# Performance work log

Measured on AMD Instinct MI355X. Metric: run time of the kernel, lower is better.

The kernel has to match this reference:

```python
import jax, jax.numpy as jnp
import numpy as np

D_MODEL = 1024
N_HEADS = 16
D_HEAD = D_MODEL // N_HEADS
RANK = 128
N_COMPRESS = 64
STATE_DIM = 64
B_SZ = 2
S_LEN = 2048


def setup_inputs() -> dict:
    key = jax.random.key(0)
    ks = jax.random.split(key, 12)
    x = jax.random.normal(ks[0], (B_SZ, S_LEN, D_MODEL), dtype=jnp.float32)
    A = jax.random.normal(ks[1], (STATE_DIM, STATE_DIM), dtype=jnp.float32) * 0.01
    B_ssm = jax.random.normal(ks[2], (D_MODEL, STATE_DIM), dtype=jnp.float32) * 0.01
    W_imp = jax.random.normal(ks[3], (D_MODEL, STATE_DIM), dtype=jnp.float32) * 0.02   # Linear(state_dim->d_model), weight [out,in]
    W_router = jax.random.normal(ks[4], (N_COMPRESS, D_MODEL), dtype=jnp.float32) * 0.02
    compress_neurons = jax.random.normal(ks[5], (N_COMPRESS, D_MODEL, RANK), dtype=jnp.float32) * 0.02
    Wq = jax.random.normal(ks[6], (D_MODEL, RANK), dtype=jnp.float32) * 0.02
    Wk = jax.random.normal(ks[7], (D_MODEL, RANK), dtype=jnp.float32) * 0.02
    Wv = jax.random.normal(ks[8], (D_MODEL, RANK), dtype=jnp.float32) * 0.02
    Wo = jax.random.normal(ks[9], (D_MODEL, D_MODEL), dtype=jnp.float32) * 0.02
    mask = jnp.tril(jnp.ones((S_LEN, S_LEN), dtype=bool))[None, None]  # [1,1,S,S] causal
    return {"x": x, "A": A, "B_ssm": B_ssm, "W_imp": W_imp, "W_router": W_router,
            "compress_neurons": compress_neurons, "Wq": Wq, "Wk": Wk, "Wv": Wv,
            "Wo": Wo, "mask": mask}


def reference(x, A, B_ssm, W_imp, W_router, compress_neurons, Wq, Wk, Wv, Wo, mask):
    Bn, S, D = x.shape
    # ---- SSM: h_t = h_{t-1} @ A + x_t @ B (only final state is used) ----
    xB = jnp.einsum('bsd,dn->bsn', x, B_ssm)  # precompute input projection

    def step(h, u):
        h = h @ A + u
        return h, None

    h0 = jnp.zeros((Bn, STATE_DIM), dtype=x.dtype)
    h_final, _ = jax.lax.scan(step, h0, jnp.swapaxes(xB, 0, 1))  # scan over S

    h_proj = h_final @ W_imp.T                       # [B, d_model]
    importance = jax.nn.softmax(jnp.einsum('bsd,bd->bs', x, h_proj), axis=-1)

    # ---- Routing ----
    token_pref = jax.nn.softmax(x @ W_router.T, axis=-1)          # [B,S,n_compress]
    nw = jnp.einsum('bs,bsn->bn', importance, token_pref)         # [B,n_compress]
    nw = nw / (nw.sum(axis=-1, keepdims=True) + 1e-8)

    # ---- Shared compression -> QKV ----
    shared_compress = jnp.einsum('bn,ndr->bdr', nw, compress_neurons)  # [B,D,rank]
    hcomp = jnp.einsum('bsd,bdr->bsr', x, shared_compress)             # [B,S,rank]
    Q = (hcomp @ Wq.T).reshape(Bn, S, N_HEADS, D_HEAD).transpose(0, 2, 1, 3)
    K = (hcomp @ Wk.T).reshape(Bn, S, N_HEADS, D_HEAD).transpose(0, 2, 1, 3)
    V = (hcomp @ Wv.T).reshape(Bn, S, N_HEADS, D_HEAD).transpose(0, 2, 1, 3)

    scores = jnp.einsum('bhqd,bhkd->bhqk', Q, K) / np.sqrt(D_HEAD).astype(x.dtype)
    scores = jnp.where(mask, scores, jnp.array(-jnp.inf, dtype=scores.dtype))
    attn = jax.nn.softmax(scores, axis=-1)
    attn_out = jnp.einsum('bhqk,bhkd->bhqd', attn, V)
    attn_out = attn_out.transpose(0, 2, 1, 3).reshape(Bn, S, D_MODEL)
    output = attn_out @ Wo.T
    return output
```

## Files before the change

### kernel.cpp

```cpp
#include <hip/hip_runtime.h>
#include <hip/hip_bf16.h>

typedef __bf16 bf16x8 __attribute__((ext_vector_type(8)));
typedef float  f32x4  __attribute__((ext_vector_type(4)));
typedef float  f32x16 __attribute__((ext_vector_type(16)));
typedef unsigned int uint4v __attribute__((ext_vector_type(4)));

__device__ __forceinline__ unsigned short f2bf(float f){
  union { float f; unsigned int u; } v; v.f = f;
  unsigned int r = (v.u + 0x7FFFu + ((v.u >> 16) & 1u)) >> 16;
  return (unsigned short)r;
}

__device__ __forceinline__ float bf2f(unsigned short u){
  union { unsigned int i; float f; } v; v.i = ((unsigned int)u) << 16; return v.f;
}

__device__ __forceinline__ unsigned pkbf(float a, float b){
  unsigned r;
  asm("v_cvt_pk_bf16_f32 %0, %1, %2" : "=v"(r) : "v"(a), "v"(b));
  return r;
}

__device__ __forceinline__ void gload_lds16(const void* g, void* l){
  __builtin_amdgcn_global_load_lds(
      (const __attribute__((address_space(1))) unsigned int*)g,
      (__attribute__((address_space(3))) unsigned int*)l, 16, 0, 0);
}

#define MFMA16(a,b,c) __builtin_amdgcn_mfma_f32_16x16x32_bf16((a),(b),(c),0,0,0)
#define MFMA32(a,b,c) __builtin_amdgcn_mfma_f32_32x32x16_bf16((a),(b),(c),0,0,0)

__global__ void k_conv(const float* __restrict__ x,
                       const float* __restrict__ Wq, const float* __restrict__ Wk,
                       const float* __restrict__ Wv, const float* __restrict__ Wo,
                       const float* __restrict__ Wr, const float* __restrict__ Bs,
                       unsigned short* __restrict__ xb16,
                       unsigned short* __restrict__ wqkv, unsigned short* __restrict__ wo,
                       unsigned short* __restrict__ wrt, float* __restrict__ xbt){
  int bid = blockIdx.x;
  if (bid >= 5632){
    int bb = (bid - 5632) >> 5, t = (bid - 5632) & 31;
    int tid = threadIdx.x, n = tid & 63, p = tid >> 6;
    const float* xr = x + ((long)bb * 2048 + 2016 + t) * 1024 + p * 256;
    const float* Bp = Bs + (p * 256) * 64 + n;
    float a0 = 0.f, a1 = 0.f, a2 = 0.f, a3 = 0.f;
    #pragma unroll 4
    for (int d = 0; d < 256; d += 4){
      float4 xv = *reinterpret_cast<const float4*>(xr + d);
      a0 += xv.x * Bp[(d    ) * 64];
      a1 += xv.y * Bp[(d + 1) * 64];
      a2 += xv.z * Bp[(d + 2) * 64];
      a3 += xv.w * Bp[(d + 3) * 64];
    }
    __shared__ float red[4][64];
    red[p][n] = (a0 + a1) + (a2 + a3);
    __syncthreads();
    if (tid < 64){
      float s = red[0][tid] + red[1][tid] + red[2][tid] + red[3][tid];
      xbt[(bb * 32 + t) * 64 + tid] = s;
    }
    return;
  }
  if (bid < 4096){
    int i = (bid * 256 + threadIdx.x) * 4;
    float4 v = *reinterpret_cast<const float4*>(x + i);
    ushort4 r; r.x = f2bf(v.x); r.y = f2bf(v.y); r.z = f2bf(v.z); r.w = f2bf(v.w);
    *reinterpret_cast<ushort4*>(xb16 + i) = r;
    return;
  }
  int j = ((bid - 4096) * 256 + threadIdx.x) * 4;
  if (j < 393216){
    const float* s;
    if (j < 131072) s = Wq + j; else if (j < 262144) s = Wk + (j - 131072); else s = Wv + (j - 262144);
    float4 v = *reinterpret_cast<const float4*>(s);
    ushort4 r; r.x = f2bf(v.x); r.y = f2bf(v.y); r.z = f2bf(v.z); r.w = f2bf(v.w);
    *reinterpret_cast<ushort4*>(wqkv + j) = r;
  } else if (j < 1441792){
    int jj = j - 393216;
    float4 v = *reinterpret_cast<const float4*>(Wo + jj);
    ushort4 r; r.x = f2bf(v.x); r.y = f2bf(v.y); r.z = f2bf(v.z); r.w = f2bf(v.w);
    *reinterpret_cast<ushort4*>(wo + jj) = r;
  } else {
    int jj = j - 1441792;
    int n = jj >> 10, d = jj & 1023;
    ushort4 r;
    if (n < 64){
      float4 v = *reinterpret_cast<const float4*>(Wr + n * 1024 + d);
      r.x = f2bf(v.x); r.y = f2bf(v.y); r.z = f2bf(v.z); r.w = f2bf(v.w);
    } else { r.x = 0; r.y = 0; r.z = 0; r.w = 0; }
    *reinterpret_cast<ushort4*>(wrt + jj) = r;
  }
}

template<int CBF16>
__global__ __launch_bounds__(256) void k_gemm(
    const unsigned short* __restrict__ A, const unsigned short* __restrict__ Bt,
    void* __restrict__ Cv, int M, int N, int K,
    long sA, long sB, long sC)
{
  __shared__ __align__(16) unsigned short Al[128 * 64];
  __shared__ __align__(16) unsigned short Bl[128 * 64];
  const int tid = threadIdx.x, wv = tid >> 6, lane = tid & 63;
  const int bm = blockIdx.y * 128, bn = blockIdx.x * 128, z = blockIdx.z;
  const unsigned short* Ab = A + (long)z * sA;
  const unsigned short* Bb = Bt + (long)z * sB;
  const f32x4 zero = {0.f, 0.f, 0.f, 0.f};
  f32x4 acc[4][4];
  #pragma unroll
  for (int i = 0; i < 4; ++i)
    #pragma unroll
    for (int j = 0; j < 4; ++j) acc[i][j] = zero;
  const int mo = (wv & 1) * 64, no = (wv >> 1) * 64;

  for (int k0 = 0; k0 < K; k0 += 64){
    __syncthreads();
    #pragma unroll
    for (int i = 0; i < 4; ++i){
      int rr = (wv * 4 + i) * 8 + (lane >> 3);
      gload_lds16(Ab + (long)(bm + rr) * K + k0 + (lane & 7) * 8, &Al[(wv * 4 + i) * 8 * 64]);
      gload_lds16(Bb + (long)(bn + rr) * K + k0 + (lane & 7) * 8, &Bl[(wv * 4 + i) * 8 * 64]);
    }
    __syncthreads();
    #pragma unroll
    for (int ks = 0; ks < 2; ++ks){
      bf16x8 af[4], bfr[4];
      #pragma unroll
      for (int mi = 0; mi < 4; ++mi)
        af[mi] = *reinterpret_cast<const bf16x8*>(&Al[(mo + mi * 16 + (lane & 15)) * 64 + ks * 32 + (lane >> 4) * 8]);
      #pragma unroll
      for (int ni = 0; ni < 4; ++ni)
        bfr[ni] = *reinterpret_cast<const bf16x8*>(&Bl[(no + ni * 16 + (lane & 15)) * 64 + ks * 32 + (lane >> 4) * 8]);
      #pragma unroll
      for (int mi = 0; mi < 4; ++mi)
        #pragma unroll
        for (int ni = 0; ni < 4; ++ni)
          acc[mi][ni] = MFMA16(af[mi], bfr[ni], acc[mi][ni]);
    }
  }

  #pragma unroll
  for (int mi = 0; mi < 4; ++mi)
    #pragma unroll
    for (int ni = 0; ni < 4; ++ni)
      #pragma unroll
      for (int r = 0; r < 4; ++r){
        int row = bm + mo + mi * 16 + (lane >> 4) * 4 + r;
        int col = bn + no + ni * 16 + (lane & 15);
        float v = acc[mi][ni][r];
        if (CBF16) ((unsigned short*)Cv)[(long)z * sC + (long)row * N + col] = f2bf(v);
        else       ((float*)Cv)[(long)z * sC + (long)row * N + col] = v;
      }
}

__global__ __launch_bounds__(256) void k_gemm64(
    const unsigned short* __restrict__ A, const unsigned short* __restrict__ Bt,
    float* __restrict__ C, int M, int N, int K)
{
  __shared__ __align__(16) unsigned short Al[128 * 64];
  __shared__ __align__(16) unsigned short Bl[64 * 64];
  const int tid = threadIdx.x, wv = tid >> 6, lane = tid & 63;
  const int bm = blockIdx.y * 128, bn = blockIdx.x * 64;
  const f32x4 zero = {0.f, 0.f, 0.f, 0.f};
  f32x4 acc[4][2];
  #pragma unroll
  for (int i = 0; i < 4; ++i){ acc[i][0] = zero; acc[i][1] = zero; }
  const int mo = (wv & 1) * 64, no = (wv >> 1) * 32;

  for (int k0 = 0; k0 < K; k0 += 64){
    __syncthreads();
    #pragma unroll
    for (int i = 0; i < 4; ++i){
      int rr = (wv * 4 + i) * 8 + (lane >> 3);
      gload_lds16(A + (long)(bm + rr) * K + k0 + (lane & 7) * 8, &Al[(wv * 4 + i) * 8 * 64]);
    }
    #pragma unroll
    for (int i = 0; i < 2; ++i){
      int rr = (wv * 2 + i) * 8 + (lane >> 3);
      gload_lds16(Bt + (long)(bn + rr) * K + k0 + (lane & 7) * 8, &Bl[(wv * 2 + i) * 8 * 64]);
    }
    __syncthreads();
    #pragma unroll
    for (int ks = 0; ks < 2; ++ks){
      bf16x8 af[4], bfr[2];
      #pragma unroll
      for (int mi = 0; mi < 4; ++mi)
        af[mi] = *reinterpret_cast<const bf16x8*>(&Al[(mo + mi * 16 + (lane & 15)) * 64 + ks * 32 + (lane >> 4) * 8]);
      #pragma unroll
      for (int ni = 0; ni < 2; ++ni)
        bfr[ni] = *reinterpret_cast<const bf16x8*>(&Bl[(no + ni * 16 + (lane & 15)) * 64 + ks * 32 + (lane >> 4) * 8]);
      #pragma unroll
      for (int mi = 0; mi < 4; ++mi)
        #pragma unroll
        for (int ni = 0; ni < 2; ++ni)
          acc[mi][ni] = MFMA16(af[mi], bfr[ni], acc[mi][ni]);
    }
  }

  #pragma unroll
  for (int mi = 0; mi < 4; ++mi)
    #pragma unroll
    for (int ni = 0; ni < 2; ++ni)
      #pragma unroll
      for (int r = 0; r < 4; ++r){
        int row = bm + mo + mi * 16 + (lane >> 4) * 4 + r;
        int col = bn + no + ni * 16 + (lane & 15);
        C[(long)row * N + col] = acc[mi][ni][r];
      }
}

__global__ __launch_bounds__(256) void k_gemmsk(
    const unsigned short* __restrict__ A, const unsigned short* __restrict__ Bt,
    float* __restrict__ P, int M, int N, int Kfull, int KS,
    long sA, long sB,
    int do_scan, const float* __restrict__ xbt, const float* __restrict__ Asc,
    float* __restrict__ hfin)
{
  __shared__ __align__(16) unsigned short Al[128 * 64];
  __shared__ __align__(16) unsigned short Bl[128 * 64];
  const int tid = threadIdx.x, wv = tid >> 6, lane = tid & 63;

  if (do_scan && blockIdx.z == 4){
    if (blockIdx.y < 2 && tid < 64){
      int b = blockIdx.y, j = tid;
      float Ac[64];
      #pragma unroll
      for (int i = 0; i < 64; ++i) Ac[i] = Asc[i * 64 + j];
      float* xs = (float*)Al;
      float* hs = xs + 2048;
      #pragma unroll
      for (int t = 0; t < 32; ++t) xs[t * 64 + j] = xbt[(b * 32 + t) * 64 + j];
      hs[j] = xs[j];
      for (int t = 1; t < 32; ++t){
        float a0 = 0.f, a1 = 0.f, a2 = 0.f, a3 = 0.f;
        #pragma unroll
        for (int ii = 0; ii < 16; ++ii){
          float4 h4 = *reinterpret_cast<const float4*>(&hs[ii * 4]);
          a0 += h4.x * Ac[ii * 4 + 0];
          a1 += h4.y * Ac[ii * 4 + 1];
          a2 += h4.z * Ac[ii * 4 + 2];
          a3 += h4.w * Ac[ii * 4 + 3];
        }
        hs[j] = (a0 + a1) + (a2 + a3) + xs[t * 64 + j];
      }
      hfin[b * 64 + j] = hs[j];
    }
    return;
  }

  const int bm = blockIdx.y * 128, bn = blockIdx.x * 128, z = blockIdx.z;
  const int b = z >> 2, s = z & 3;
  const unsigned short* Ab = A + (long)b * sA;
  const unsigned short* Bb = Bt + (long)b * sB;
  float* Pb = P + (long)z * M * N;
  const f32x4 zero = {0.f, 0.f, 0.f, 0.f};
  f32x4 acc[4][4];
  #pragma unroll
  for (int i = 0; i < 4; ++i)
    #pragma unroll
    for (int j = 0; j < 4; ++j) acc[i][j] = zero;
  const int mo = (wv & 1) * 64, no = (wv >> 1) * 64;

  const int k1 = s * KS + KS;
  for (int k0 = s * KS; k0 < k1; k0 += 64){
    __syncthreads();
    #pragma unroll
    for (int i = 0; i < 4; ++i){
      int rr = (wv * 4 + i) * 8 + (lane >> 3);
      gload_lds16(Ab + (long)(bm + rr) * Kfull + k0 + (lane & 7) * 8, &Al[(wv * 4 + i) * 8 * 64]);
      gload_lds16(Bb + (long)(bn + rr) * Kfull + k0 + (lane & 7) * 8, &Bl[(wv * 4 + i) * 8 * 64]);
    }
    __syncthreads();
    #pragma unroll
    for (int ks = 0; ks < 2; ++ks){
      bf16x8 af[4], bfr[4];
      #pragma unroll
      for (int mi = 0; mi < 4; ++mi)
        af[mi] = *reinterpret_cast<const bf16x8*>(&Al[(mo + mi * 16 + (lane & 15)) * 64 + ks * 32 + (lane >> 4) * 8]);
      #pragma unroll
      for (int ni = 0; ni < 4; ++ni)
        bfr[ni] = *reinterpret_cast<const bf16x8*>(&Bl[(no + ni * 16 + (lane & 15)) * 64 + ks * 32 + (lane >> 4) * 8]);
      #pragma unroll
      for (int mi = 0; mi < 4; ++mi)
        #pragma unroll
        for (int ni = 0; ni < 4; ++ni)
          acc[mi][ni] = MFMA16(af[mi], bfr[ni], acc[mi][ni]);
    }
  }

  #pragma unroll
  for (int mi = 0; mi < 4; ++mi)
    #pragma unroll
    for (int ni = 0; ni < 4; ++ni)
      #pragma unroll
      for (int r = 0; r < 4; ++r){
        int row = bm + mo + mi * 16 + (lane >> 4) * 4 + r;
        int col = bn + no + ni * 16 + (lane & 15);
        Pb[(long)row * N + col] = acc[mi][ni][r];
      }
}

__global__ __launch_bounds__(256) void k_hred(const float* __restrict__ hpp,
                                              unsigned short* __restrict__ hcomp){
  int i4 = (blockIdx.x * 256 + threadIdx.x) * 4;
  int b = i4 >> 18;
  int rem = i4 & 262143;
  const float* p = hpp + (long)(b * 4) * 262144 + rem;
  f32x4 v = *reinterpret_cast<const f32x4*>(p);
  v += *reinterpret_cast<const f32x4*>(p + 262144);
  v += *reinterpret_cast<const f32x4*>(p + 524288);
  v += *reinterpret_cast<const f32x4*>(p + 786432);
  ushort4 o; o.x = f2bf(v[0]); o.y = f2bf(v[1]); o.z = f2bf(v[2]); o.w = f2bf(v[3]);
  *reinterpret_cast<ushort4*>(hcomp + (long)b * 262144 + rem) = o;
}

__global__ __launch_bounds__(256) void k_hproj(const float* __restrict__ hfin,
                                               const float* __restrict__ Wimp,
                                               float* __restrict__ hproj){
  int bid = blockIdx.x;
  int b = bid >> 2;
  int d = (bid & 3) * 256 + threadIdx.x;
  __shared__ float hs[64];
  if (threadIdx.x < 64) hs[threadIdx.x] = hfin[b * 64 + threadIdx.x];
  __syncthreads();
  const float* wr = Wimp + (long)d * 64;
  float a0 = 0.f, a1 = 0.f, a2 = 0.f, a3 = 0.f;
  #pragma unroll
  for (int k = 0; k < 64; k += 4){
    float4 w4 = *reinterpret_cast<const float4*>(wr + k);
    float4 h4 = *reinterpret_cast<const float4*>(&hs[k]);
    a0 += w4.x * h4.x; a1 += w4.y * h4.y; a2 += w4.z * h4.z; a3 += w4.w * h4.w;
  }
  hproj[b * 1024 + d] = (a0 + a1) + (a2 + a3);
}

__global__ void k_logits(const float* __restrict__ x, const float* __restrict__ hproj,
                         float* __restrict__ l){
  int tid = threadIdx.x, lane = tid & 63, wv = tid >> 6;
  int rowbase = blockIdx.x * 16;
  int b = rowbase >> 11;
  float hp[16];
  #pragma unroll
  for (int i = 0; i < 16; ++i) hp[i] = hproj[b * 1024 + i * 64 + lane];
  for (int rr = 0; rr < 4; ++rr){
    int row = rowbase + wv * 4 + rr;
    const float* xr = x + (long)row * 1024;
    float acc = 0.f;
    #pragma unroll
    for (int i = 0; i < 16; ++i) acc += xr[i * 64 + lane] * hp[i];
    #pragma unroll
    for (int o = 32; o; o >>= 1) acc += __shfl_xor(acc, o, 64);
    if (lane == 0) l[row] = acc;
  }
}

__global__ void k_nwpart(const float* __restrict__ rpp, const float* __restrict__ lbuf,
                         float* __restrict__ nwp){
  int bid = blockIdx.x; int b = bid >> 4, chunk = bid & 15;
  int tid = threadIdx.x, wv = tid >> 6, lane = tid & 63;
  __shared__ float wred[4], wsum[4];
  __shared__ float red[4][64];
  const float* lr = lbuf + b * 2048;
  float4 va = *reinterpret_cast<const float4*>(lr + tid * 8);
  float4 vb = *reinterpret_cast<const float4*>(lr + tid * 8 + 4);
  float mx8 = fmaxf(fmaxf(fmaxf(va.x, va.y), fmaxf(va.z, va.w)),
                    fmaxf(fmaxf(vb.x, vb.y), fmaxf(vb.z, vb.w)));
  #pragma unroll
  for (int o = 32; o; o >>= 1) mx8 = fmaxf(mx8, __shfl_xor(mx8, o, 64));
  if (lane == 0) wred[wv] = mx8;
  __syncthreads();
  float M = fmaxf(fmaxf(wred[0], wred[1]), fmaxf(wred[2], wred[3]));
  float se = __expf(va.x - M) + __expf(va.y - M) + __expf(va.z - M) + __expf(va.w - M)
           + __expf(vb.x - M) + __expf(vb.y - M) + __expf(vb.z - M) + __expf(vb.w - M);
  #pragma unroll
  for (int o = 32; o; o >>= 1) se += __shfl_xor(se, o, 64);
  if (lane == 0) wsum[wv] = se;
  __syncthreads();
  float inv = 1.f / (wsum[0] + wsum[1] + wsum[2] + wsum[3]);

  float accn = 0.f;
  for (int t = 0; t < 32; ++t){
    int s = chunk * 128 + wv * 32 + t;
    long off = ((long)b * 2048 + s) * 128 + lane;
    float v = rpp[off] + rpp[off + 524288] + rpp[off + 1048576] + rpp[off + 1572864];
    float mx = v;
    #pragma unroll
    for (int o = 32; o; o >>= 1) mx = fmaxf(mx, __shfl_xor(mx, o, 64));
    float e = __expf(v - mx);
    float sm = e;
    #pragma unroll
    for (int o = 32; o; o >>= 1) sm += __shfl_xor(sm, o, 64);
    float impv = __expf(lr[s] - M) * inv;
    accn += impv * (e / sm);
  }
  red[wv][lane] = accn;
  __syncthreads();
  if (wv == 0){
    float t = red[0][lane] + red[1][lane] + red[2][lane] + red[3][lane];
    nwp[bid * 64 + lane] = t;
  }
}

__global__ void k_sc(const float* __restrict__ cn, const float* __restrict__ nwp,
                     unsigned short* __restrict__ sct){
  int tid = threadIdx.x;
  long idx = (long)blockIdx.x * 256 + tid;
  int d = (int)(idx >> 5); int r0 = (int)(idx & 31) * 4;
  __shared__ float nws[128];
  if (tid < 128){
    int bb = tid >> 6, nn = tid & 63;
    float a = 0.f;
    #pragma unroll
    for (int c = 0; c < 16; ++c) a += nwp[(bb * 16 + c) * 64 + nn];
    float tot = a;
    #pragma unroll
    for (int o = 32; o; o >>= 1) tot += __shfl_xor(tot, o, 64);
    nws[tid] = a / (tot + 1e-8f);
  }
  __syncthreads();
  f32x4 a0 = {0.f,0.f,0.f,0.f}, a1 = {0.f,0.f,0.f,0.f};
  for (int n = 0; n < 64; ++n){
    f32x4 c = *reinterpret_cast<const f32x4*>(&cn[((long)n * 1024 + d) * 128 + r0]);
    a0 += nws[n] * c;
    a1 += nws[64 + n] * c;
  }
  #pragma unroll
  for (int e = 0; e < 4; ++e){
    sct[(long)(r0 + e) * 1024 + d]        = f2bf(a0[e]);
    sct[(long)(128 + r0 + e) * 1024 + d]  = f2bf(a1[e]);
  }
}

__global__ __launch_bounds__(256, 4) void k_attn(const unsigned short* __restrict__ qkv,
                                                 unsigned short* __restrict__ Op,
                                                 float* __restrict__ ml,
                                                 int nspl, int nsh){
  __shared__ __align__(16) unsigned short KlA[64 * 64];
  __shared__ __align__(16) unsigned short VtA[64 * 64];
  char* Kl = (char*)KlA;
  char* Vt = (char*)VtA;
  const int tid = threadIdx.x, wq = tid >> 6, lane = tid & 63;
  const int l31 = lane & 31, hi = lane >> 5;
  const float CEXP = 0.18033688011112042f;

  int li = blockIdx.x;
  int j = li & 7, m = li >> 3;
  int g = j * 4 + (m & 3);
  int r5 = m >> 2;
  int k5 = r5 & 7, sel = r5 >> 3;
  int qb = (sel < nspl) ? (15 - k5) : k5;
  int part = (sel < nspl) ? sel : (sel - nspl);
  int h = g & 15, b = g >> 4;
  int pidx = (g * 16 + qb) * nspl + part;

  int T = 2 * qb + 2;
  int t0 = (part * T) >> nsh;
  int t1 = ((part + 1) * T) >> nsh;

  int qbase = qb * 128 + wq * 32;
  int KTw = qbase >> 6;
  const unsigned short* base = qkv + (long)b * 2048 * 3072;

  bf16x8 qf[4];
  #pragma unroll
  for (int i = 0; i < 4; ++i)
    qf[i] = *reinterpret_cast<const bf16x8*>(base + (long)(qbase + l31) * 3072 + h * 64 + i * 16 + hi * 8);

  f32x16 oacc[2];
  #pragma unroll
  for (int d = 0; d < 2; ++d)
    #pragma unroll
    for (int r = 0; r < 16; ++r) oacc[d][r] = 0.f;
  float m_r = -3.0e38f, l_r = 0.f;

  for (int kt = t0; kt < t1; ++kt){
    #pragma unroll
    for (int it = 0; it < 2; ++it){
      int key = it * 32 + wq * 8 + (lane >> 3);
      int sc = (lane & 7) ^ (key & 7);
      gload_lds16(base + (long)(kt * 64 + key) * 3072 + 1024 + h * 64 + sc * 8,
                  Kl + (it * 32 + wq * 8) * 128);
    }
    #pragma unroll
    for (int it = 0; it < 2; ++it){
      int dhg = wq + it * 4;
      uint4 vvv = *reinterpret_cast<const uint4*>(base + (long)(kt * 64 + lane) * 3072 + 2048 + h * 64 + dhg * 8);
      const unsigned short* vs = reinterpret_cast<const unsigned short*>(&vvv);
      #pragma unroll
      for (int e = 0; e < 8; ++e){
        int dh = dhg * 8 + e;
        *reinterpret_cast<unsigned short*>(Vt + dh * 128 + ((((lane >> 3) ^ (dh & 7))) << 4) + (lane & 7) * 2) = vs[e];
      }
    }
    __syncthreads();

    if (kt <= KTw){
      bool diag = (kt == KTw);

      f32x16 sa[2];
      __builtin_amdgcn_s_setprio(1);
      #pragma unroll
      for (int kb = 0; kb < 2; ++kb){
        #pragma unroll
        for (int r = 0; r < 16; ++r) sa[kb][r] = 0.f;
        int row = kb * 32 + l31;
        #pragma unroll
        for (int i2 = 0; i2 < 4; ++i2){
          bf16x8 kf = *reinterpret_cast<const bf16x8*>(
              Kl + row * 128 + ((((i2 << 1) | hi) ^ (l31 & 7)) << 4));
          sa[kb] = MFMA32(kf, qf[i2], sa[kb]);
        }
      }
      __builtin_amdgcn_s_setprio(0);

      float pv[32];
      #pragma unroll
      for (int kb = 0; kb < 2; ++kb)
        #pragma unroll
        for (int r = 0; r < 16; ++r) pv[kb * 16 + r] = sa[kb][r];

      if (diag){
        int qg = qbase + l31;
        #pragma unroll
        for (int kb = 0; kb < 2; ++kb)
          #pragma unroll
          for (int r = 0; r < 16; ++r){
            int kg = kt * 64 + kb * 32 + (r & 3) + ((r >> 2) << 3) + (hi << 2);
            if (kg > qg) pv[kb * 16 + r] = -3.0e38f;
          }
      }

      float mt[16];
      #pragma unroll
      for (int r = 0; r < 16; ++r) mt[r] = fmaxf(pv[r], pv[r + 16]);
      #pragma unroll
      for (int r = 0; r < 8; ++r) mt[r] = fmaxf(mt[r], mt[r + 8]);
      #pragma unroll
      for (int r = 0; r < 4; ++r) mt[r] = fmaxf(mt[r], mt[r + 4]);
      float mx = fmaxf(fmaxf(mt[0], mt[1]), fmaxf(mt[2], mt[3]));
      mx = fmaxf(mx, __shfl_xor(mx, 32, 64));

      float scl;
      if (__all(mx <= m_r + 44.0f)){
        scl = 1.f;
      } else {
        float mnew = fmaxf(m_r, mx);
        scl = exp2f((m_r - mnew) * CEXP);
        m_r = mnew;
        #pragma unroll
        for (int d = 0; d < 2; ++d)
          #pragma unroll
          for (int r = 0; r < 16; ++r) oacc[d][r] *= scl;
      }
      float mn_c = m_r * CEXP;
      float rs0 = 0.f, rs1 = 0.f, rs2 = 0.f, rs3 = 0.f;
      #pragma unroll
      for (int r = 0; r < 32; r += 4){
        float e0 = exp2f(__builtin_fmaf(pv[r    ], CEXP, -mn_c)); pv[r    ] = e0; rs0 += e0;
        float e1 = exp2f(__builtin_fmaf(pv[r + 1], CEXP, -mn_c)); pv[r + 1] = e1; rs1 += e1;
        float e2 = exp2f(__builtin_fmaf(pv[r + 2], CEXP, -mn_c)); pv[r + 2] = e2; rs2 += e2;
        float e3 = exp2f(__builtin_fmaf(pv[r + 3], CEXP, -mn_c)); pv[r + 3] = e3; rs3 += e3;
      }
      float rs = (rs0 + rs1) + (rs2 + rs3);
      rs += __shfl_xor(rs, 32, 64);
      l_r = l_r * scl + rs;

      bf16x8 pa[4];
      #pragma unroll
      for (int kb = 0; kb < 2; ++kb){
        unsigned W[4][2], X[4][2];
        #pragma unroll
        for (int u = 0; u < 4; ++u){
          W[u][0] = pkbf(pv[kb * 16 + 4 * u + 0], pv[kb * 16 + 4 * u + 1]);
          W[u][1] = pkbf(pv[kb * 16 + 4 * u + 2], pv[kb * 16 + 4 * u + 3]);
        }
        #pragma unroll
        for (int u = 0; u < 4; ++u){
          X[u][0] = (unsigned)__shfl_xor((int)W[u][0], 32, 64);
          X[u][1] = (unsigned)__shfl_xor((int)W[u][1], 32, 64);
        }
        #pragma unroll
        for (int t2 = 0; t2 < 2; ++t2){
          int u0 = 2 * t2, u1 = u0 + 1;
          uint4v wt;
          wt.x = hi ? X[u1][0] : W[u0][0];
          wt.y = hi ? X[u1][1] : W[u0][1];
          wt.z = hi ? W[u1][0] : X[u0][0];
          wt.w = hi ? W[u1][1] : X[u0][1];
          pa[kb * 2 + t2] = __builtin_bit_cast(bf16x8, wt);
        }
      }
      __builtin_amdgcn_s_setprio(1);
      #pragma unroll
      for (int db = 0; db < 2; ++db){
        int row = db * 32 + l31;
        #pragma unroll
        for (int t = 0; t < 4; ++t){
          bf16x8 vf = *reinterpret_cast<const bf16x8*>(
              Vt + row * 128 + ((((t << 1) | hi) ^ (l31 & 7)) << 4));
          oacc[db] = MFMA32(vf, pa[t], oacc[db]);
        }
      }
      __builtin_amdgcn_s_setprio(0);
    }
    __syncthreads();
  }

  unsigned short* Oq = Op + (long)pidx * 8192 + (wq * 32 + l31) * 64;
  #pragma unroll
  for (int db = 0; db < 2; ++db)
    #pragma unroll
    for (int r4 = 0; r4 < 4; ++r4){
      ushort4 o;
      o.x = f2bf(oacc[db][r4 * 4 + 0]);
      o.y = f2bf(oacc[db][r4 * 4 + 1]);
      o.z = f2bf(oacc[db][r4 * 4 + 2]);
      o.w = f2bf(oacc[db][r4 * 4 + 3]);
      *reinterpret_cast<ushort4*>(Oq + db * 32 + r4 * 8 + hi * 4) = o;
    }
  if (hi == 0){
    float2 v; v.x = m_r; v.y = l_r;
    *reinterpret_cast<float2*>(ml + ((long)pidx * 128 + wq * 32 + l31) * 2) = v;
  }
}

__global__ __launch_bounds__(256) void k_amerge(const unsigned short* __restrict__ Op,
                                                const float* __restrict__ ml,
                                                unsigned short* __restrict__ ao,
                                                int nspl){
  const float CEXP = 0.18033688011112042f;
  int mid = blockIdx.x >> 1;
  int hh = blockIdx.x & 1;
  int g = mid >> 4, qb = mid & 15;
  int b = g >> 4, h = g & 15;
  const unsigned short* O0 = Op + (long)mid * nspl * 8192;
  const float* mlb = ml + (long)mid * nspl * 256;
  int t = threadIdx.x;
  #pragma unroll
  for (int i = 0; i < 4; ++i){
    int idx = hh * 1024 + i * 256 + t;
    int q = idx >> 4, c4 = (idx & 15) * 4;
    float m0 = mlb[q * 2],       l0 = mlb[q * 2 + 1];
    float m1 = mlb[256 + q * 2], l1 = mlb[256 + q * 2 + 1];
    float m2 = -3.0e38f, l2 = 0.f, m3 = -3.0e38f, l3 = 0.f;
    if (nspl == 4){
      m2 = mlb[512 + q * 2]; l2 = mlb[512 + q * 2 + 1];
      m3 = mlb[768 + q * 2]; l3 = mlb[768 + q * 2 + 1];
    }
    float mm = fmaxf(fmaxf(m0, m1), fmaxf(m2, m3));
    float s0 = exp2f((m0 - mm) * CEXP), s1 = exp2f((m1 - mm) * CEXP);
    float s2 = exp2f((m2 - mm) * CEXP), s3 = exp2f((m3 - mm) * CEXP);
    float linv = 1.f / (l0 * s0 + l1 * s1 + l2 * s2 + l3 * s3);
    s0 *= linv; s1 *= linv; s2 *= linv; s3 *= linv;
    ushort4 a = *reinterpret_cast<const ushort4*>(O0 + q * 64 + c4);
    ushort4 c = *reinterpret_cast<const ushort4*>(O0 + 8192 + q * 64 + c4);
    ushort4 a2 = {0,0,0,0}, a3 = {0,0,0,0};
    if (nspl == 4){
      a2 = *reinterpret_cast<const ushort4*>(O0 + 16384 + q * 64 + c4);
      a3 = *reinterpret_cast<const ushort4*>(O0 + 24576 + q * 64 + c4);
    }
    ushort4 o;
    o.x = f2bf(bf2f(a.x) * s0 + bf2f(c.x) * s1 + bf2f(a2.x) * s2 + bf2f(a3.x) * s3);
    o.y = f2bf(bf2f(a.y) * s0 + bf2f(c.y) * s1 + bf2f(a2.y) * s2 + bf2f(a3.y) * s3);
    o.z = f2bf(bf2f(a.z) * s0 + bf2f(c.z) * s1 + bf2f(a2.z) * s2 + bf2f(a3.z) * s3);
    o.w = f2bf(bf2f(a.w) * s0 + bf2f(c.w) * s1 + bf2f(a2.w) * s2 + bf2f(a3.w) * s3);
    *reinterpret_cast<ushort4*>(ao + ((long)b * 2048 + qb * 128 + q) * 1024 + h * 64 + c4) = o;
  }
}

extern "C" void kernel_launch(void* const* d_in, const int* in_sizes, int n_in,
                              void* d_out, int out_size, void* d_ws, size_t ws_size,
                              hipStream_t stream){
  (void)in_sizes; (void)n_in; (void)out_size;
  const float* x    = (const float*)d_in[0];
  const float* A    = (const float*)d_in[1];
  const float* Bs   = (const float*)d_in[2];
  const float* Wimp = (const float*)d_in[3];
  const float* Wr   = (const float*)d_in[4];
  const float* cn   = (const float*)d_in[5];
  const float* Wq   = (const float*)d_in[6];
  const float* Wk   = (const float*)d_in[7];
  const float* Wv   = (const float*)d_in[8];
  const float* Wo   = (const float*)d_in[9];
  float* out = (float*)d_out;
  char* ws = (char*)d_ws;

  int nspl, nsh;
  {
    size_t tot4 = (size_t)512*4*16384 + (size_t)512*4*1024 + 25165824 + 2097152 + 2800000;
    if (ws_size >= tot4){ nspl = 4; nsh = 2; } else { nspl = 2; nsh = 1; }
  }
  size_t opart_b = (size_t)512 * nspl * 16384;
  size_t ml_off  = opart_b;
  size_t qkv_off = ml_off + (size_t)512 * nspl * 1024;
  size_t wo_off  = qkv_off + 25165824;
  size_t ext     = wo_off + 2097152;

  unsigned short* Opart = (unsigned short*)(ws);
  float*          mlbuf = (float*)(ws + ml_off);
  unsigned short* qkvb  = (unsigned short*)(ws + qkv_off);
  float*          hpp   = (float*)(ws + qkv_off);
  unsigned short* aob   = (unsigned short*)(ws + qkv_off);
  unsigned short* wo_t  = (unsigned short*)(ws + wo_off);
  unsigned short* xb16  = (unsigned short*)(ws + 0);
  float*          rpp   = (float*)(ws + 8388608);
  unsigned short* sct   = (unsigned short*)(ws + ext);
  float*          xbt   = (float*)(ws + ext + 524288);
  float*          hproj = (float*)(ws + ext + 540672);
  float*          lbuf  = (float*)(ws + ext + 548864);
  float*          nwp   = (float*)(ws + ext + 565248);
  float*          hfin  = (float*)(ws + ext + 573440);
  unsigned short* wqkv  = (unsigned short*)(ws + ext + 577536);
  unsigned short* wrt   = (unsigned short*)(ws + ext + 1363968);
  unsigned short* hcomp = (unsigned short*)(ws + ext + 1626112);

  k_conv<<<5696, 256, 0, stream>>>(x, Wq, Wk, Wv, Wo, Wr, Bs, xb16, wqkv, wo_t, wrt, xbt);
  k_gemmsk<<<dim3(1, 32, 5), 256, 0, stream>>>(xb16, wrt, rpp, 4096, 128, 1024, 256, 0, 0,
                                               1, xbt, A, hfin);
  k_hproj<<<8, 256, 0, stream>>>(hfin, Wimp, hproj);
  k_logits<<<256, 256, 0, stream>>>(x, hproj, lbuf);
  k_nwpart<<<32, 256, 0, stream>>>(rpp, lbuf, nwp);
  k_sc<<<128, 256, 0, stream>>>(cn, nwp, sct);
  k_gemmsk<<<dim3(1, 16, 8), 256, 0, stream>>>(xb16, sct, hpp, 2048, 128, 1024, 256,
                                               2048L * 1024, 128L * 1024, 0, nullptr, nullptr, nullptr);
  k_hred<<<512, 256, 0, stream>>>(hpp, hcomp);
  k_gemm<1><<<dim3(24, 16, 2), 256, 0, stream>>>(hcomp, wqkv, qkvb, 2048, 3072, 128,
                                                 2048L * 128, 0, 2048L * 3072);
  k_attn<<<dim3(512 * nspl), 256, 0, stream>>>(qkvb, Opart, mlbuf, nspl, nsh);
  k_amerge<<<dim3(1024), 256, 0, stream>>>(Opart, mlbuf, aob, nspl);
  k_gemm64<<<dim3(16, 32), 256, 0, stream>>>(aob, wo_t, out, 4096, 1024, 1024);
}
```

Measured before the change: 169.4 us.

## Fuse hproj into logits kernel and double attention query tile to 256 rows

Removes the separate k_hproj launch: every k_logits block now recomputes h_proj for its batch from hfin and W_imp into shared memory. The attention kernel moves from 256-thread blocks covering 128 queries to 512-thread blocks covering 256 queries (8 waves), so each K/V tile load into LDS is shared by twice as many queries and the partial-output and merge indexing is rescaled to match. The trade-offs are redundant h_proj work in all 256 logits blocks, fewer and larger attention blocks with coarser causal load balance, and more register pressure under launch_bounds(512,4).

```diff
diff --git a/kernel.cpp b/kernel.cpp
--- a/kernel.cpp
+++ b/kernel.cpp
@@ -314,34 +314,34 @@
   *reinterpret_cast<ushort4*>(hcomp + (long)b * 262144 + rem) = o;
 }
 
-__global__ __launch_bounds__(256) void k_hproj(const float* __restrict__ hfin,
-                                               const float* __restrict__ Wimp,
-                                               float* __restrict__ hproj){
-  int bid = blockIdx.x;
-  int b = bid >> 2;
-  int d = (bid & 3) * 256 + threadIdx.x;
-  __shared__ float hs[64];
-  if (threadIdx.x < 64) hs[threadIdx.x] = hfin[b * 64 + threadIdx.x];
-  __syncthreads();
-  const float* wr = Wimp + (long)d * 64;
-  float a0 = 0.f, a1 = 0.f, a2 = 0.f, a3 = 0.f;
-  #pragma unroll
-  for (int k = 0; k < 64; k += 4){
-    float4 w4 = *reinterpret_cast<const float4*>(wr + k);
-    float4 h4 = *reinterpret_cast<const float4*>(&hs[k]);
-    a0 += w4.x * h4.x; a1 += w4.y * h4.y; a2 += w4.z * h4.z; a3 += w4.w * h4.w;
-  }
-  hproj[b * 1024 + d] = (a0 + a1) + (a2 + a3);
-}
-
-__global__ void k_logits(const float* __restrict__ x, const float* __restrict__ hproj,
-                         float* __restrict__ l){
+__global__ __launch_bounds__(256) void k_logits(const float* __restrict__ x,
+                                                const float* __restrict__ hfin,
+                                                const float* __restrict__ Wimp,
+                                                float* __restrict__ l){
   int tid = threadIdx.x, lane = tid & 63, wv = tid >> 6;
   int rowbase = blockIdx.x * 16;
   int b = rowbase >> 11;
+  __shared__ float hs[64];
+  __shared__ float hpl[1024];
+  if (tid < 64) hs[tid] = hfin[b * 64 + tid];
+  __syncthreads();
+  #pragma unroll
+  for (int e = 0; e < 4; ++e){
+    int d = tid * 4 + e;
+    const float* wr = Wimp + (long)d * 64;
+    float a0 = 0.f, a1 = 0.f, a2 = 0.f, a3 = 0.f;
+    #pragma unroll
+    for (int k = 0; k < 64; k += 4){
+      float4 w4 = *reinterpret_cast<const float4*>(wr + k);
+      float4 h4 = *reinterpret_cast<const float4*>(&hs[k]);
+      a0 += w4.x * h4.x; a1 += w4.y * h4.y; a2 += w4.z * h4.z; a3 += w4.w * h4.w;
+    }
+    hpl[d] = (a0 + a1) + (a2 + a3);
+  }
+  __syncthreads();
   float hp[16];
   #pragma unroll
-  for (int i = 0; i < 16; ++i) hp[i] = hproj[b * 1024 + i * 64 + lane];
+  for (int i = 0; i < 16; ++i) hp[i] = hpl[i * 64 + lane];
   for (int rr = 0; rr < 4; ++rr){
     int row = rowbase + wv * 4 + rr;
     const float* xr = x + (long)row * 1024;
@@ -431,7 +431,7 @@
   }
 }
 
-__global__ __launch_bounds__(256, 4) void k_attn(const unsigned short* __restrict__ qkv,
+__global__ __launch_bounds__(512, 4) void k_attn(const unsigned short* __restrict__ qkv,
                                                  unsigned short* __restrict__ Op,
                                                  float* __restrict__ ml,
                                                  int nspl, int nsh){
@@ -439,7 +439,7 @@
   __shared__ __align__(16) unsigned short VtA[64 * 64];
   char* Kl = (char*)KlA;
   char* Vt = (char*)VtA;
-  const int tid = threadIdx.x, wq = tid >> 6, lane = tid & 63;
+  const int tid = threadIdx.x, w = tid >> 6, lane = tid & 63;
   const int l31 = lane & 31, hi = lane >> 5;
   const float CEXP = 0.18033688011112042f;
 
@@ -447,17 +447,17 @@
   int j = li & 7, m = li >> 3;
   int g = j * 4 + (m & 3);
   int r5 = m >> 2;
-  int k5 = r5 & 7, sel = r5 >> 3;
-  int qb = (sel < nspl) ? (15 - k5) : k5;
+  int k5 = r5 & 3, sel = r5 >> 2;
+  int qpair = (sel < nspl) ? (7 - k5) : k5;
   int part = (sel < nspl) ? sel : (sel - nspl);
   int h = g & 15, b = g >> 4;
-  int pidx = (g * 16 + qb) * nspl + part;
-
-  int T = 2 * qb + 2;
+  int pidx = (g * 8 + qpair) * nspl + part;
+
+  int T = 4 * qpair + 4;
   int t0 = (part * T) >> nsh;
   int t1 = ((part + 1) * T) >> nsh;
 
-  int qbase = qb * 128 + wq * 32;
+  int qbase = qpair * 256 + w * 32;
   int KTw = qbase >> 6;
   const unsigned short* base = qkv + (long)b * 2048 * 3072;
 
@@ -474,21 +474,16 @@
   float m_r = -3.0e38f, l_r = 0.f;
 
   for (int kt = t0; kt < t1; ++kt){
-    #pragma unroll
-    for (int it = 0; it < 2; ++it){
-      int key = it * 32 + wq * 8 + (lane >> 3);
-      int sc = (lane & 7) ^ (key & 7);
+    {
+      int key = w * 8 + (lane >> 3);
+      int sc = (lane & 7) ^ (lane >> 3);
       gload_lds16(base + (long)(kt * 64 + key) * 3072 + 1024 + h * 64 + sc * 8,
-                  Kl + (it * 32 + wq * 8) * 128);
-    }
-    #pragma unroll
-    for (int it = 0; it < 2; ++it){
-      int dhg = wq + it * 4;
-      uint4 vvv = *reinterpret_cast<const uint4*>(base + (long)(kt * 64 + lane) * 3072 + 2048 + h * 64 + dhg * 8);
+                  Kl + (w * 8) * 128);
+      uint4 vvv = *reinterpret_cast<const uint4*>(base + (long)(kt * 64 + lane) * 3072 + 2048 + h * 64 + w * 8);
       const unsigned short* vs = reinterpret_cast<const unsigned short*>(&vvv);
       #pragma unroll
       for (int e = 0; e < 8; ++e){
-        int dh = dhg * 8 + e;
+        int dh = w * 8 + e;
         *reinterpret_cast<unsigned short*>(Vt + dh * 128 + ((((lane >> 3) ^ (dh & 7))) << 4) + (lane & 7) * 2) = vs[e];
       }
     }
@@ -606,7 +601,7 @@
     __syncthreads();
   }
 
-  unsigned short* Oq = Op + (long)pidx * 8192 + (wq * 32 + l31) * 64;
+  unsigned short* Oq = Op + (long)pidx * 16384 + (w * 32 + l31) * 64;
   #pragma unroll
   for (int db = 0; db < 2; ++db)
     #pragma unroll
@@ -620,7 +615,7 @@
     }
   if (hi == 0){
     float2 v; v.x = m_r; v.y = l_r;
-    *reinterpret_cast<float2*>(ml + ((long)pidx * 128 + wq * 32 + l31) * 2) = v;
+    *reinterpret_cast<float2*>(ml + ((long)pidx * 256 + w * 32 + l31) * 2) = v;
   }
 }
 
@@ -629,23 +624,23 @@
                                                 unsigned short* __restrict__ ao,
                                                 int nspl){
   const float CEXP = 0.18033688011112042f;
-  int mid = blockIdx.x >> 1;
-  int hh = blockIdx.x & 1;
-  int g = mid >> 4, qb = mid & 15;
+  int mid = blockIdx.x >> 2;
+  int quarter = blockIdx.x & 3;
+  int g = mid >> 3, qpair = mid & 7;
   int b = g >> 4, h = g & 15;
-  const unsigned short* O0 = Op + (long)mid * nspl * 8192;
-  const float* mlb = ml + (long)mid * nspl * 256;
+  const unsigned short* O0 = Op + (long)mid * nspl * 16384;
+  const float* mlb = ml + (long)mid * nspl * 512;
   int t = threadIdx.x;
   #pragma unroll
   for (int i = 0; i < 4; ++i){
-    int idx = hh * 1024 + i * 256 + t;
-    int q = idx >> 4, c4 = (idx & 15) * 4;
+    int idx4 = quarter * 1024 + i * 256 + t;
+    int q = idx4 >> 4, c4 = (idx4 & 15) * 4;
     float m0 = mlb[q * 2],       l0 = mlb[q * 2 + 1];
-    float m1 = mlb[256 + q * 2], l1 = mlb[256 + q * 2 + 1];
+    float m1 = mlb[512 + q * 2], l1 = mlb[512 + q * 2 + 1];
     float m2 = -3.0e38f, l2 = 0.f, m3 = -3.0e38f, l3 = 0.f;
     if (nspl == 4){
-      m2 = mlb[512 + q * 2]; l2 = mlb[512 + q * 2 + 1];
-      m3 = mlb[768 + q * 2]; l3 = mlb[768 + q * 2 + 1];
+      m2 = mlb[1024 + q * 2]; l2 = mlb[1024 + q * 2 + 1];
+      m3 = mlb[1536 + q * 2]; l3 = mlb[1536 + q * 2 + 1];
     }
     float mm = fmaxf(fmaxf(m0, m1), fmaxf(m2, m3));
     float s0 = exp2f((m0 - mm) * CEXP), s1 = exp2f((m1 - mm) * CEXP);
@@ -653,18 +648,18 @@
     float linv = 1.f / (l0 * s0 + l1 * s1 + l2 * s2 + l3 * s3);
     s0 *= linv; s1 *= linv; s2 *= linv; s3 *= linv;
     ushort4 a = *reinterpret_cast<const ushort4*>(O0 + q * 64 + c4);
-    ushort4 c = *reinterpret_cast<const ushort4*>(O0 + 8192 + q * 64 + c4);
+    ushort4 c = *reinterpret_cast<const ushort4*>(O0 + 16384 + q * 64 + c4);
     ushort4 a2 = {0,0,0,0}, a3 = {0,0,0,0};
     if (nspl == 4){
-      a2 = *reinterpret_cast<const ushort4*>(O0 + 16384 + q * 64 + c4);
-      a3 = *reinterpret_cast<const ushort4*>(O0 + 24576 + q * 64 + c4);
+      a2 = *reinterpret_cast<const ushort4*>(O0 + 32768 + q * 64 + c4);
+      a3 = *reinterpret_cast<const ushort4*>(O0 + 49152 + q * 64 + c4);
     }
     ushort4 o;
     o.x = f2bf(bf2f(a.x) * s0 + bf2f(c.x) * s1 + bf2f(a2.x) * s2 + bf2f(a3.x) * s3);
     o.y = f2bf(bf2f(a.y) * s0 + bf2f(c.y) * s1 + bf2f(a2.y) * s2 + bf2f(a3.y) * s3);
     o.z = f2bf(bf2f(a.z) * s0 + bf2f(c.z) * s1 + bf2f(a2.z) * s2 + bf2f(a3.z) * s3);
     o.w = f2bf(bf2f(a.w) * s0 + bf2f(c.w) * s1 + bf2f(a2.w) * s2 + bf2f(a3.w) * s3);
-    *reinterpret_cast<ushort4*>(ao + ((long)b * 2048 + qb * 128 + q) * 1024 + h * 64 + c4) = o;
+    *reinterpret_cast<ushort4*>(ao + ((long)b * 2048 + qpair * 256 + q) * 1024 + h * 64 + c4) = o;
   }
 }
 
@@ -706,7 +701,6 @@
   float*          rpp   = (float*)(ws + 8388608);
   unsigned short* sct   = (unsigned short*)(ws + ext);
   float*          xbt   = (float*)(ws + ext + 524288);
-  float*          hproj = (float*)(ws + ext + 540672);
   float*          lbuf  = (float*)(ws + ext + 548864);
   float*          nwp   = (float*)(ws + ext + 565248);
   float*          hfin  = (float*)(ws + ext + 573440);
@@ -717,8 +711,7 @@
   k_conv<<<5696, 256, 0, stream>>>(x, Wq, Wk, Wv, Wo, Wr, Bs, xb16, wqkv, wo_t, wrt, xbt);
   k_gemmsk<<<dim3(1, 32, 5), 256, 0, stream>>>(xb16, wrt, rpp, 4096, 128, 1024, 256, 0, 0,
                                                1, xbt, A, hfin);
-  k_hproj<<<8, 256, 0, stream>>>(hfin, Wimp, hproj);
-  k_logits<<<256, 256, 0, stream>>>(x, hproj, lbuf);
+  k_logits<<<256, 256, 0, stream>>>(x, hfin, Wimp, lbuf);
   k_nwpart<<<32, 256, 0, stream>>>(rpp, lbuf, nwp);
   k_sc<<<128, 256, 0, stream>>>(cn, nwp, sct);
   k_gemmsk<<<dim3(1, 16, 8), 256, 0, stream>>>(xb16, sct, hpp, 2048, 128, 1024, 256,
@@ -726,7 +719,7 @@
   k_hred<<<512, 256, 0, stream>>>(hpp, hcomp);
   k_gemm<1><<<dim3(24, 16, 2), 256, 0, stream>>>(hcomp, wqkv, qkvb, 2048, 3072, 128,
                                                  2048L * 128, 0, 2048L * 3072);
-  k_attn<<<dim3(512 * nspl), 256, 0, stream>>>(qkvb, Opart, mlbuf, nspl, nsh);
+  k_attn<<<dim3(256 * nspl), 512, 0, stream>>>(qkvb, Opart, mlbuf, nspl, nsh);
   k_amerge<<<dim3(1024), 256, 0, stream>>>(Opart, mlbuf, aob, nspl);
   k_gemm64<<<dim3(16, 32), 256, 0, stream>>>(aob, wo_t, out, 4096, 1024, 1024);
 }
```

New measurement: 181.6 us. 1.07x slower.
